# Kernel optimization log

Hardware: AMD Instinct MI355X
Metric: run time of the kernel (lower is better)

Reference implementation:

```python
import jax, jax.numpy as jnp
import numpy as np

N_NODES = 100000
N_EDGES = 1600000
N_GRAPHS = 2048
D = 128
H = 128
EPS = 1e-5


def gcn_conv(x, src, dst, W, b, n):
    # x: [N, Din], W: [Din, Dout]; GCN with added self-loops and symmetric norm
    xw = x @ W                                       # [N, Dout]
    deg = jnp.zeros((n,), x.dtype).at[dst].add(1.0) + 1.0  # deg of A+I (counted on dst)
    dinv = jax.lax.rsqrt(deg)                        # [N]
    norm = dinv[src] * dinv[dst]                     # [E]
    msg = xw[src] * norm[:, None]                    # [E, Dout] gather + scale
    agg = jax.ops.segment_sum(msg, dst, num_segments=n)
    agg = agg + xw * (dinv * dinv)[:, None]          # self-loop contribution
    return agg + b


def gru_step_h0(x, W_ih, W_hh, b_ih, b_hh):
    # single GRU step with h0 = 0 (PyTorch gate order r, z, n)
    h0 = jnp.zeros_like(x)
    gi = x @ W_ih.T + b_ih                           # [G, 3H]
    gh = h0 @ W_hh.T + b_hh                          # [G, 3H] (zeros + b_hh)
    ir, iz, inn = jnp.split(gi, 3, axis=-1)
    hr, hz, hn = jnp.split(gh, 3, axis=-1)
    r = jax.nn.sigmoid(ir + hr)
    z = jax.nn.sigmoid(iz + hz)
    n = jnp.tanh(inn + r * hn)
    return (1.0 - z) * n + z * h0


def setup_inputs() -> dict:
    key = jax.random.key(0)
    ks = jax.random.split(key, 10)
    x = jax.random.normal(ks[0], (N_NODES, D), jnp.float32)
    edge_index = jax.random.randint(ks[1], (2, N_EDGES), 0, N_NODES, jnp.int32)
    batch = jnp.sort(jax.random.randint(ks[2], (N_NODES,), 0, N_GRAPHS, jnp.int32))
    s = 1.0 / np.sqrt(H)
    return {
        "x": x,
        "edge_index": edge_index,
        "batch": batch,
        "W1": jax.random.normal(ks[3], (D, H), jnp.float32) * s,
        "b1": jnp.zeros((H,), jnp.float32),
        "W2": jax.random.normal(ks[4], (H, H), jnp.float32) * s,
        "b2": jnp.zeros((H,), jnp.float32),
        "W_ih": jax.random.normal(ks[5], (3 * H, H), jnp.float32) * s,
        "W_hh": jax.random.normal(ks[6], (3 * H, H), jnp.float32) * s,
        "b_ih": jnp.zeros((3 * H,), jnp.float32),
        "b_hh": jnp.zeros((3 * H,), jnp.float32),
        "W_lin": jax.random.normal(ks[7], (1, H), jnp.float32) * s,
        "b_lin": jnp.zeros((1,), jnp.float32),
    }


def reference(x, edge_index, batch, W1, b1, W2, b2, W_ih, W_hh, b_ih, b_hh, W_lin, b_lin):
    src, dst = edge_index[0], edge_index[1]
    n = x.shape[0]
    h = jax.nn.relu(gcn_conv(x, src, dst, W1, b1, n))
    h = gcn_conv(h, src, dst, W2, b2, n)
    # global_mean_pool over graph ids
    sums = jax.ops.segment_sum(h, batch, num_segments=N_GRAPHS)
    cnts = jax.ops.segment_sum(jnp.ones((n,), h.dtype), batch, num_segments=N_GRAPHS)
    g = sums / jnp.maximum(cnts, 1.0)[:, None]       # [G, H]
    # dropout p=0.5 in eval mode -> identity
    g = gru_step_h0(g, W_ih, W_hh, b_ih, b_hh)
    g = jax.nn.relu(g)
    mu = jnp.mean(g, axis=-1, keepdims=True)
    var = jnp.mean(jnp.square(g - mu), axis=-1, keepdims=True)
    g = (g - mu) * jax.lax.rsqrt(var + EPS)          # layer_norm, no affine
    return g @ W_lin.T + b_lin                       # [G, 1]
```

## Files before the change

kernel.cpp:

```cpp
#include <hip/hip_runtime.h>
#include <hip/hip_bf16.h>
#include <math.h>

#define DHID 128
#define SH 8
#define BIN_T 8192
#define CAPSH 13

typedef __attribute__((ext_vector_type(8))) short bf16x8;
typedef __attribute__((ext_vector_type(4))) float f32x4;

__device__ __forceinline__ int atomAddI(int* p, int v) {
    return __hip_atomic_fetch_add(p, v, __ATOMIC_RELAXED, __HIP_MEMORY_SCOPE_AGENT);
}
__device__ __forceinline__ float bf_lo(unsigned u) { return __uint_as_float(u << 16); }
__device__ __forceinline__ float bf_hi(unsigned u) { return __uint_as_float(u & 0xffff0000u); }
__device__ __forceinline__ float bf_us(unsigned short u) { return __uint_as_float((unsigned)u << 16); }
__device__ __forceinline__ unsigned short bf16_1(float f) {
    unsigned u = __float_as_uint(f);
    u += 0x7fffu + ((u >> 16) & 1u);
    return (unsigned short)(u >> 16);
}
__device__ __forceinline__ unsigned pack_bf16x2(float a, float b) {
    unsigned ua = __float_as_uint(a);
    unsigned ub = __float_as_uint(b);
    ua = (ua + 0x7fffu + ((ua >> 16) & 1u)) >> 16;
    ub = (ub + 0x7fffu + ((ub >> 16) & 1u)) & 0xffff0000u;
    return ua | ub;
}

__global__ __launch_bounds__(256) void bin_edges(const int* __restrict__ src,
                                                 const int* __restrict__ dst,
                                                 int* __restrict__ bcur,
                                                 unsigned* __restrict__ staged,
                                                 int E, int NB) {
    __shared__ int lh[512], lbase[512], lcur[512];
    int t = threadIdx.x;
    int e0 = blockIdx.x * BIN_T;
    int eend = min(e0 + BIN_T, E);
    for (int i = t; i < NB; i += 256) { lh[i] = 0; lcur[i] = 0; }
    __syncthreads();
    for (int e = e0 + t; e < eend; e += 256)
        atomicAdd(&lh[dst[e] >> SH], 1);
    __syncthreads();
    for (int i = t; i < NB; i += 256)
        lbase[i] = lh[i] ? atomAddI(&bcur[i], lh[i]) : 0;
    __syncthreads();
    for (int e = e0 + t; e < eend; e += 256) {
        int d = dst[e];
        int b = d >> SH;
        int pos = lbase[b] + atomicAdd(&lcur[b], 1);
        staged[((size_t)b << CAPSH) + pos] =
            (unsigned)src[e] | ((unsigned)(d & ((1 << SH) - 1)) << 24);
    }
}

__global__ __launch_bounds__(512) void scan_weights(const int* __restrict__ bcur,
                                                    int* __restrict__ gboff,
                                                    int* __restrict__ off,
                                                    const float* __restrict__ W1,
                                                    const float* __restrict__ W2,
                                                    const float* __restrict__ Wih,
                                                    unsigned short* __restrict__ Wt1,
                                                    unsigned short* __restrict__ Wt2,
                                                    unsigned short* __restrict__ Wihb,
                                                    int N, int E, int NB) {
    int t = threadIdx.x;
    if (blockIdx.x == 0) {
        __shared__ int sh[512];
        int v = (t < NB) ? bcur[t] : 0;
        sh[t] = v;
        __syncthreads();
#pragma unroll
        for (int o = 1; o < 512; o <<= 1) {
            int x = (t >= o) ? sh[t - o] : 0;
            __syncthreads();
            sh[t] += x;
            __syncthreads();
        }
        if (t < NB) gboff[t] = sh[t] - v;
        if (t == 0) { gboff[NB] = E; off[N] = E; }
    } else {
        int idx = (blockIdx.x - 1) * 512 + t;
        if (idx < 16384) {
            int k = idx >> 7, n = idx & 127;
            Wt1[n * 128 + k] = bf16_1(W1[idx]);
        } else if (idx < 32768) {
            int j = idx - 16384;
            int k = j >> 7, n = j & 127;
            Wt2[n * 128 + k] = bf16_1(W2[j]);
        } else if (idx < 32768 + 49152) {
            int j = idx - 32768;
            Wihb[j] = bf16_1(Wih[j]);
        }
    }
}

__global__ __launch_bounds__(256) void scatter_csr(const unsigned* __restrict__ staged,
                                                   const int* __restrict__ bcur,
                                                   const int* __restrict__ gboff,
                                                   int* __restrict__ off,
                                                   float* __restrict__ dinv,
                                                   int* __restrict__ rec, int N) {
    __shared__ int sh[256];
    __shared__ int curs[256];
    __shared__ int hist[256];
    int t = threadIdx.x;
    int b = blockIdx.x;
    int node0 = b << SH;
    int cnt_b = bcur[b];
    int base = gboff[b];
    const unsigned* st = staged + ((size_t)b << CAPSH);
    hist[t] = 0;
    __syncthreads();
    for (int j = t; j < cnt_b; j += 256)
        atomicAdd(&hist[st[j] >> 24], 1);
    __syncthreads();
    int v = hist[t];
    sh[t] = v;
    __syncthreads();
#pragma unroll
    for (int o = 1; o < 256; o <<= 1) {
        int x = (t >= o) ? sh[t - o] : 0;
        __syncthreads();
        sh[t] += x;
        __syncthreads();
    }
    int excl = sh[t] - v;
    int node = node0 + t;
    if (node < N) {
        off[node] = base + excl;
        dinv[node] = rsqrtf((float)v + 1.0f);
    }
    curs[t] = base + excl;
    __syncthreads();
    for (int j = t; j < cnt_b; j += 256) {
        unsigned w = st[j];
        int dl = w >> 24;
        int pos = atomicAdd(&curs[dl], 1);
        rec[pos] = (int)(w & 0xFFFFFFu);
    }
}

__global__ __launch_bounds__(256) void gemm_mfma(const void* __restrict__ Xv,
                                                 const unsigned short* __restrict__ Wt,
                                                 unsigned short* __restrict__ Y,
                                                 int N, int x_is_bf16,
                                                 int wstride, int ystride) {
    __shared__ unsigned short Xs[64 * 136];
    __shared__ unsigned short Ws[128 * 136];
    const int tid = threadIdx.x;
    const unsigned short* Wg = Wt + (size_t)blockIdx.y * wstride;
    unsigned short* Yg = Y + (size_t)blockIdx.y * ystride;

    {
        const uint4* W4 = (const uint4*)Wg;
#pragma unroll
        for (int i = 0; i < 8; i++) {
            int idx = tid + i * 256;
            int r = idx >> 4, c8 = idx & 15;
            *(uint4*)&Ws[r * 136 + c8 * 8] = W4[idx];
        }
    }
    const int row0 = blockIdx.x * 64;
    if (x_is_bf16) {
        const uint4* X4 = (const uint4*)Xv;
#pragma unroll
        for (int i = 0; i < 4; i++) {
            int idx = tid + i * 256;
            int r = idx >> 4, c8 = idx & 15;
            uint4 v = make_uint4(0u, 0u, 0u, 0u);
            if (row0 + r < N) v = X4[(size_t)(row0 + r) * 16 + c8];
            *(uint4*)&Xs[r * 136 + c8 * 8] = v;
        }
    } else {
        const float4* X4 = (const float4*)Xv;
#pragma unroll
        for (int i = 0; i < 8; i++) {
            int idx = tid + i * 256;
            int r = idx >> 5, c4 = idx & 31;
            float4 v = make_float4(0.f, 0.f, 0.f, 0.f);
            if (row0 + r < N) v = X4[(size_t)(row0 + r) * 32 + c4];
            uint2 pk = make_uint2(pack_bf16x2(v.x, v.y), pack_bf16x2(v.z, v.w));
            *(uint2*)&Xs[r * 136 + c4 * 4] = pk;
        }
    }
    __syncthreads();

    const int lane = tid & 63;
    const int wv = tid >> 6;
    const int m = lane & 15, quad = lane >> 4;
    const int wrow = wv * 16;

    f32x4 acc[8];
#pragma unroll
    for (int i = 0; i < 8; i++) acc[i] = (f32x4){0.f, 0.f, 0.f, 0.f};

#pragma unroll
    for (int kc = 0; kc < 4; kc++) {
        bf16x8 a = *(const bf16x8*)&Xs[(wrow + m) * 136 + kc * 32 + quad * 8];
#pragma unroll
        for (int nt = 0; nt < 8; nt++) {
            bf16x8 b = *(const bf16x8*)&Ws[(nt * 16 + m) * 136 + kc * 32 + quad * 8];
            acc[nt] = __builtin_amdgcn_mfma_f32_16x16x32_bf16(a, b, acc[nt], 0, 0, 0);
        }
    }

#pragma unroll
    for (int r = 0; r < 4; r++) {
        int row = row0 + wrow + quad * 4 + r;
        if (row < N) {
#pragma unroll
            for (int nt = 0; nt < 8; nt++) {
                Yg[(size_t)row * DHID + nt * 16 + m] = bf16_1(acc[nt][r]);
            }
        }
    }
}

__global__ __launch_bounds__(256) void aggregate(const unsigned short* __restrict__ A,
                                                 const float* __restrict__ dinv,
                                                 const int* __restrict__ off,
                                                 const int* __restrict__ rec,
                                                 const float* __restrict__ bias,
                                                 void* __restrict__ Bout, int N, int mode) {
    int node = blockIdx.x * 4 + (threadIdx.x >> 6);
    if (node >= N) return;
    int lane = threadIdx.x & 63;
    int q  = lane >> 4;
    int ql = lane & 15;
    float di = dinv[node];
    float acc[8];
    if (q == 0) {
        float s = di * di;
        uint4 v = ((const uint4*)(A + (size_t)node * DHID))[ql];
        const float4* bb = (const float4*)(bias + ql * 8);
        float4 b0 = bb[0], b1 = bb[1];
        acc[0] = bf_lo(v.x) * s + b0.x;
        acc[1] = bf_hi(v.x) * s + b0.y;
        acc[2] = bf_lo(v.y) * s + b0.z;
        acc[3] = bf_hi(v.y) * s + b0.w;
        acc[4] = bf_lo(v.z) * s + b1.x;
        acc[5] = bf_hi(v.z) * s + b1.y;
        acc[6] = bf_lo(v.w) * s + b1.z;
        acc[7] = bf_hi(v.w) * s + b1.w;
    } else {
#pragma unroll
        for (int i = 0; i < 8; i++) acc[i] = 0.f;
    }
    int j = off[node] + q;
    int jend = off[node + 1];
    for (; j + 4 < jend; j += 8) {
        int s0 = rec[j];
        int s1 = rec[j + 4];
        uint4 v0 = ((const uint4*)(A + (size_t)s0 * DHID))[ql];
        uint4 v1 = ((const uint4*)(A + (size_t)s1 * DHID))[ql];
        float w0 = dinv[s0] * di;
        float w1 = dinv[s1] * di;
        acc[0] += bf_lo(v0.x) * w0 + bf_lo(v1.x) * w1;
        acc[1] += bf_hi(v0.x) * w0 + bf_hi(v1.x) * w1;
        acc[2] += bf_lo(v0.y) * w0 + bf_lo(v1.y) * w1;
        acc[3] += bf_hi(v0.y) * w0 + bf_hi(v1.y) * w1;
        acc[4] += bf_lo(v0.z) * w0 + bf_lo(v1.z) * w1;
        acc[5] += bf_hi(v0.z) * w0 + bf_hi(v1.z) * w1;
        acc[6] += bf_lo(v0.w) * w0 + bf_lo(v1.w) * w1;
        acc[7] += bf_hi(v0.w) * w0 + bf_hi(v1.w) * w1;
    }
    if (j < jend) {
        int s0 = rec[j];
        uint4 v0 = ((const uint4*)(A + (size_t)s0 * DHID))[ql];
        float w0 = dinv[s0] * di;
        acc[0] += bf_lo(v0.x) * w0;
        acc[1] += bf_hi(v0.x) * w0;
        acc[2] += bf_lo(v0.y) * w0;
        acc[3] += bf_hi(v0.y) * w0;
        acc[4] += bf_lo(v0.z) * w0;
        acc[5] += bf_hi(v0.z) * w0;
        acc[6] += bf_lo(v0.w) * w0;
        acc[7] += bf_hi(v0.w) * w0;
    }
#pragma unroll
    for (int i = 0; i < 8; i++) {
        acc[i] += __shfl_xor(acc[i], 16);
        acc[i] += __shfl_xor(acc[i], 32);
    }
    if (q == 0) {
        if (mode == 1) {
            uint4 pk;
            pk.x = pack_bf16x2(fmaxf(acc[0], 0.f), fmaxf(acc[1], 0.f));
            pk.y = pack_bf16x2(fmaxf(acc[2], 0.f), fmaxf(acc[3], 0.f));
            pk.z = pack_bf16x2(fmaxf(acc[4], 0.f), fmaxf(acc[5], 0.f));
            pk.w = pack_bf16x2(fmaxf(acc[6], 0.f), fmaxf(acc[7], 0.f));
            ((uint4*)((unsigned short*)Bout + (size_t)node * DHID))[ql] = pk;
        } else {
            float4* bp = (float4*)((float*)Bout + (size_t)node * DHID) + ql * 2;
            bp[0] = make_float4(acc[0], acc[1], acc[2], acc[3]);
            bp[1] = make_float4(acc[4], acc[5], acc[6], acc[7]);
        }
    }
}

__global__ __launch_bounds__(256) void pool_mean(const float* __restrict__ B,
                                                 const int* __restrict__ batch,
                                                 float* __restrict__ g, int N, int G) {
    __shared__ int se[2];
    __shared__ float red[128];
    const int t = threadIdx.x;
    const int gr = blockIdx.x;
    if (t < 2) {
        int target = gr + t, lo = 0, hi = N;
        while (lo < hi) {
            int mid = (lo + hi) >> 1;
            if (batch[mid] < target) lo = mid + 1; else hi = mid;
        }
        se[t] = lo;
    }
    __syncthreads();
    const int s = se[0], e = se[1];
    const int col = t & 127, rh = t >> 7;
    float sum = 0.f;
    for (int r = s + rh; r < e; r += 2) sum += B[(size_t)r * DHID + col];
    if (rh == 1) red[col] = sum;
    __syncthreads();
    if (rh == 0) {
        float tot = sum + red[col];
        g[(size_t)gr * DHID + col] = tot / fmaxf((float)(e - s), 1.0f);
    }
}

__global__ __launch_bounds__(128) void gate_ln_head(const unsigned short* __restrict__ gi,
                                                    const float* __restrict__ b_ih,
                                                    const float* __restrict__ b_hh,
                                                    const float* __restrict__ W_lin,
                                                    const float* __restrict__ b_lin,
                                                    float* __restrict__ out, int G) {
    __shared__ float red[2];
    const int t = threadIdx.x;
    const int g = blockIdx.x;

    float d0 = bf_us(gi[(size_t)g * DHID + t]);
    float d1 = bf_us(gi[(size_t)(G + g) * DHID + t]);
    float d2 = bf_us(gi[(size_t)(2 * G + g) * DHID + t]);

    float rg = 1.f / (1.f + expf(-(d0 + b_ih[t] + b_hh[t])));
    float zg = 1.f / (1.f + expf(-(d1 + b_ih[128 + t] + b_hh[128 + t])));
    float ng = tanhf(d2 + b_ih[256 + t] + rg * b_hh[256 + t]);
    float y = fmaxf((1.f - zg) * ng, 0.f);

    auto blockSum = [&](float v) -> float {
#pragma unroll
        for (int o = 1; o < 64; o <<= 1) v += __shfl_xor(v, o);
        __syncthreads();
        if ((t & 63) == 0) red[t >> 6] = v;
        __syncthreads();
        return red[0] + red[1];
    };

    float mu = blockSum(y) * (1.f / 128.f);
    float dy = y - mu;
    float var = blockSum(dy * dy) * (1.f / 128.f);
    float yn = dy * rsqrtf(var + 1e-5f);
    float tot = blockSum(yn * W_lin[t]);
    if (t == 0) out[g] = tot + b_lin[0];
}

extern "C" void kernel_launch(void* const* d_in, const int* in_sizes, int n_in,
                              void* d_out, int out_size, void* d_ws, size_t ws_size,
                              hipStream_t stream) {
    const float* x     = (const float*)d_in[0];
    const int*   ei    = (const int*)d_in[1];
    const int*   batch = (const int*)d_in[2];
    const float* W1    = (const float*)d_in[3];
    const float* b1    = (const float*)d_in[4];
    const float* W2    = (const float*)d_in[5];
    const float* b2    = (const float*)d_in[6];
    const float* W_ih  = (const float*)d_in[7];
    const float* b_ih  = (const float*)d_in[9];
    const float* b_hh  = (const float*)d_in[10];
    const float* W_lin = (const float*)d_in[11];
    const float* b_lin = (const float*)d_in[12];
    float* out = (float*)d_out;

    const int N = in_sizes[0] / DHID;
    const int E = in_sizes[1] / 2;
    const int G = out_size;
    const int* src = ei;
    const int* dst = ei + E;
    const int NB = (N + (1 << SH) - 1) >> SH;

    auto align256 = [](size_t v) { return (v + 255) & ~(size_t)255; };
    char* p = (char*)d_ws;
    size_t used = 0;
    auto carve = [&](size_t bytes) -> char* {
        char* q = p + used;
        used += align256(bytes);
        return q;
    };

    int*   off    = (int*)carve(((size_t)N + 1) * 4);
    int*   bcur   = (int*)carve(512 * 4);
    int*   gboff  = (int*)carve(513 * 4);
    float* dinv   = (float*)carve((size_t)N * 4);
    unsigned* staged = (unsigned*)carve(((size_t)NB << CAPSH) * 4);
    int*   rec    = (int*)carve((size_t)E * 4);
    float* gbuf   = (float*)carve((size_t)G * DHID * 4);
    unsigned short* Wt1  = (unsigned short*)carve((size_t)128 * 128 * 2);
    unsigned short* Wt2  = (unsigned short*)carve((size_t)128 * 128 * 2);
    unsigned short* Wihb = (unsigned short*)carve((size_t)3 * 128 * 128 * 2);
    unsigned short* gib  = (unsigned short*)carve((size_t)3 * G * DHID * 2);
    unsigned short* A    = (unsigned short*)carve((size_t)N * DHID * 2);
    unsigned short* B1b  = (unsigned short*)carve((size_t)N * DHID * 2);
    size_t matB = (size_t)N * DHID * sizeof(float);
    float* B2f;
    if (ws_size >= used + matB) {
        B2f = (float*)carve(matB);
    } else {
        B2f = (float*)d_in[0];
    }

    dim3 blk(256);
    int nb_g  = (N + 63) / 64;
    int nb_ag = (N + 3) / 4;
    int nb_bin = (E + BIN_T - 1) / BIN_T;
    int nb_wp  = (81920 + 511) / 512;

    hipMemsetAsync(bcur, 0, (size_t)NB * 4, stream);
    bin_edges<<<nb_bin, blk, 0, stream>>>(src, dst, bcur, staged, E, NB);
    scan_weights<<<1 + nb_wp, dim3(512), 0, stream>>>(bcur, gboff, off,
                                                      W1, W2, W_ih, Wt1, Wt2, Wihb,
                                                      N, E, NB);
    scatter_csr<<<NB, blk, 0, stream>>>(staged, bcur, gboff, off, dinv, rec, N);

    gemm_mfma<<<dim3(nb_g, 1), blk, 0, stream>>>(x, Wt1, A, N, 0, 0, 0);
    aggregate<<<nb_ag, blk, 0, stream>>>(A, dinv, off, rec, b1, B1b, N, 1);

    gemm_mfma<<<dim3(nb_g, 1), blk, 0, stream>>>(B1b, Wt2, A, N, 1, 0, 0);
    aggregate<<<nb_ag, blk, 0, stream>>>(A, dinv, off, rec, b2, B2f, N, 0);

    pool_mean<<<G, blk, 0, stream>>>(B2f, batch, gbuf, N, G);
    gemm_mfma<<<dim3((G + 63) / 64, 3), blk, 0, stream>>>(gbuf, Wihb, gib, G, 0,
                                                          128 * 128, G * DHID);
    gate_ln_head<<<G, dim3(128), 0, stream>>>(gib, b_ih, b_hh, W_lin, b_lin, out, G);
}
```

Measured before the change: 364.7 us.

## Fuse bin/scan kernels, stage GEMM stores via LDS, store layer-2 output as bf16

```diff
diff --git a/kernel.cpp b/kernel.cpp
--- a/kernel.cpp
+++ b/kernel.cpp
@@ -33,55 +33,16 @@
                                                  const int* __restrict__ dst,
                                                  int* __restrict__ bcur,
                                                  unsigned* __restrict__ staged,
-                                                 int E, int NB) {
-    __shared__ int lh[512], lbase[512], lcur[512];
+                                                 const float* __restrict__ W1,
+                                                 const float* __restrict__ W2,
+                                                 const float* __restrict__ Wih,
+                                                 unsigned short* __restrict__ Wt1,
+                                                 unsigned short* __restrict__ Wt2,
+                                                 unsigned short* __restrict__ Wihb,
+                                                 int E, int NB, int nb_bin) {
     int t = threadIdx.x;
-    int e0 = blockIdx.x * BIN_T;
-    int eend = min(e0 + BIN_T, E);
-    for (int i = t; i < NB; i += 256) { lh[i] = 0; lcur[i] = 0; }
-    __syncthreads();
-    for (int e = e0 + t; e < eend; e += 256)
-        atomicAdd(&lh[dst[e] >> SH], 1);
-    __syncthreads();
-    for (int i = t; i < NB; i += 256)
-        lbase[i] = lh[i] ? atomAddI(&bcur[i], lh[i]) : 0;
-    __syncthreads();
-    for (int e = e0 + t; e < eend; e += 256) {
-        int d = dst[e];
-        int b = d >> SH;
-        int pos = lbase[b] + atomicAdd(&lcur[b], 1);
-        staged[((size_t)b << CAPSH) + pos] =
-            (unsigned)src[e] | ((unsigned)(d & ((1 << SH) - 1)) << 24);
-    }
-}
-
-__global__ __launch_bounds__(512) void scan_weights(const int* __restrict__ bcur,
-                                                    int* __restrict__ gboff,
-                                                    int* __restrict__ off,
-                                                    const float* __restrict__ W1,
-                                                    const float* __restrict__ W2,
-                                                    const float* __restrict__ Wih,
-                                                    unsigned short* __restrict__ Wt1,
-                                                    unsigned short* __restrict__ Wt2,
-                                                    unsigned short* __restrict__ Wihb,
-                                                    int N, int E, int NB) {
-    int t = threadIdx.x;
-    if (blockIdx.x == 0) {
-        __shared__ int sh[512];
-        int v = (t < NB) ? bcur[t] : 0;
-        sh[t] = v;
-        __syncthreads();
-#pragma unroll
-        for (int o = 1; o < 512; o <<= 1) {
-            int x = (t >= o) ? sh[t - o] : 0;
-            __syncthreads();
-            sh[t] += x;
-            __syncthreads();
-        }
-        if (t < NB) gboff[t] = sh[t] - v;
-        if (t == 0) { gboff[NB] = E; off[N] = E; }
-    } else {
-        int idx = (blockIdx.x - 1) * 512 + t;
+    if (blockIdx.x >= nb_bin) {
+        int idx = (blockIdx.x - nb_bin) * 256 + t;
         if (idx < 16384) {
             int k = idx >> 7, n = idx & 127;
             Wt1[n * 128 + k] = bf16_1(W1[idx]);
@@ -93,26 +54,55 @@
             int j = idx - 32768;
             Wihb[j] = bf16_1(Wih[j]);
         }
+        return;
+    }
+    __shared__ int lh[512], lbase[512], lcur[512];
+    int e0 = blockIdx.x * BIN_T;
+    int eend = min(e0 + BIN_T, E);
+    for (int i = t; i < NB; i += 256) { lh[i] = 0; lcur[i] = 0; }
+    __syncthreads();
+    for (int e = e0 + t; e < eend; e += 256)
+        atomicAdd(&lh[dst[e] >> SH], 1);
+    __syncthreads();
+    for (int i = t; i < NB; i += 256)
+        lbase[i] = lh[i] ? atomAddI(&bcur[i], lh[i]) : 0;
+    __syncthreads();
+    for (int e = e0 + t; e < eend; e += 256) {
+        int d = dst[e];
+        int b = d >> SH;
+        int pos = lbase[b] + atomicAdd(&lcur[b], 1);
+        staged[((size_t)b << CAPSH) + pos] =
+            (unsigned)src[e] | ((unsigned)(d & ((1 << SH) - 1)) << 24);
     }
 }
 
 __global__ __launch_bounds__(256) void scatter_csr(const unsigned* __restrict__ staged,
                                                    const int* __restrict__ bcur,
-                                                   const int* __restrict__ gboff,
                                                    int* __restrict__ off,
                                                    float* __restrict__ dinv,
-                                                   int* __restrict__ rec, int N) {
+                                                   int* __restrict__ rec,
+                                                   int N, int E, int NB) {
     __shared__ int sh[256];
     __shared__ int curs[256];
     __shared__ int hist[256];
     int t = threadIdx.x;
     int b = blockIdx.x;
     int node0 = b << SH;
+
+    int s0 = (t < b) ? bcur[t] : 0;
+    int s1 = (256 + t < b) ? bcur[256 + t] : 0;
+    int s = s0 + s1;
+#pragma unroll
+    for (int o = 1; o < 64; o <<= 1) s += __shfl_xor(s, o);
+    if ((t & 63) == 0) sh[t >> 6] = s;
+    __syncthreads();
+    int base = sh[0] + sh[1] + sh[2] + sh[3];
+    __syncthreads();
+
+    hist[t] = 0;
+    __syncthreads();
     int cnt_b = bcur[b];
-    int base = gboff[b];
     const unsigned* st = staged + ((size_t)b << CAPSH);
-    hist[t] = 0;
-    __syncthreads();
     for (int j = t; j < cnt_b; j += 256)
         atomicAdd(&hist[st[j] >> 24], 1);
     __syncthreads();
@@ -132,6 +122,7 @@
         off[node] = base + excl;
         dinv[node] = rsqrtf((float)v + 1.0f);
     }
+    if (b == NB - 1 && t == 0) off[N] = E;
     curs[t] = base + excl;
     __syncthreads();
     for (int j = t; j < cnt_b; j += 256) {
@@ -208,13 +199,19 @@
 
 #pragma unroll
     for (int r = 0; r < 4; r++) {
-        int row = row0 + wrow + quad * 4 + r;
-        if (row < N) {
-#pragma unroll
-            for (int nt = 0; nt < 8; nt++) {
-                Yg[(size_t)row * DHID + nt * 16 + m] = bf16_1(acc[nt][r]);
-            }
-        }
+        int lrow = wrow + quad * 4 + r;
+#pragma unroll
+        for (int nt = 0; nt < 8; nt++)
+            Xs[lrow * 136 + nt * 16 + m] = bf16_1(acc[nt][r]);
+    }
+    __syncthreads();
+#pragma unroll
+    for (int i = 0; i < 4; i++) {
+        int idx = tid + i * 256;
+        int r = idx >> 4, c8 = idx & 15;
+        if (row0 + r < N)
+            *(uint4*)&Yg[(size_t)(row0 + r) * DHID + c8 * 8] =
+                *(const uint4*)&Xs[r * 136 + c8 * 8];
     }
 }
 
@@ -223,7 +220,8 @@
                                                  const int* __restrict__ off,
                                                  const int* __restrict__ rec,
                                                  const float* __restrict__ bias,
-                                                 void* __restrict__ Bout, int N, int mode) {
+                                                 unsigned short* __restrict__ Bout,
+                                                 int N, int mode) {
     int node = blockIdx.x * 4 + (threadIdx.x >> 6);
     if (node >= N) return;
     int lane = threadIdx.x & 63;
@@ -286,21 +284,19 @@
     }
     if (q == 0) {
         if (mode == 1) {
-            uint4 pk;
-            pk.x = pack_bf16x2(fmaxf(acc[0], 0.f), fmaxf(acc[1], 0.f));
-            pk.y = pack_bf16x2(fmaxf(acc[2], 0.f), fmaxf(acc[3], 0.f));
-            pk.z = pack_bf16x2(fmaxf(acc[4], 0.f), fmaxf(acc[5], 0.f));
-            pk.w = pack_bf16x2(fmaxf(acc[6], 0.f), fmaxf(acc[7], 0.f));
-            ((uint4*)((unsigned short*)Bout + (size_t)node * DHID))[ql] = pk;
-        } else {
-            float4* bp = (float4*)((float*)Bout + (size_t)node * DHID) + ql * 2;
-            bp[0] = make_float4(acc[0], acc[1], acc[2], acc[3]);
-            bp[1] = make_float4(acc[4], acc[5], acc[6], acc[7]);
-        }
-    }
-}
-
-__global__ __launch_bounds__(256) void pool_mean(const float* __restrict__ B,
+#pragma unroll
+            for (int i = 0; i < 8; i++) acc[i] = fmaxf(acc[i], 0.f);
+        }
+        uint4 pk;
+        pk.x = pack_bf16x2(acc[0], acc[1]);
+        pk.y = pack_bf16x2(acc[2], acc[3]);
+        pk.z = pack_bf16x2(acc[4], acc[5]);
+        pk.w = pack_bf16x2(acc[6], acc[7]);
+        ((uint4*)(Bout + (size_t)node * DHID))[ql] = pk;
+    }
+}
+
+__global__ __launch_bounds__(256) void pool_mean(const unsigned short* __restrict__ B,
                                                  const int* __restrict__ batch,
                                                  float* __restrict__ g, int N, int G) {
     __shared__ int se[2];
@@ -319,7 +315,7 @@
     const int s = se[0], e = se[1];
     const int col = t & 127, rh = t >> 7;
     float sum = 0.f;
-    for (int r = s + rh; r < e; r += 2) sum += B[(size_t)r * DHID + col];
+    for (int r = s + rh; r < e; r += 2) sum += bf_us(B[(size_t)r * DHID + col]);
     if (rh == 1) red[col] = sum;
     __syncthreads();
     if (rh == 0) {
@@ -399,7 +395,6 @@
 
     int*   off    = (int*)carve(((size_t)N + 1) * 4);
     int*   bcur   = (int*)carve(512 * 4);
-    int*   gboff  = (int*)carve(513 * 4);
     float* dinv   = (float*)carve((size_t)N * 4);
     unsigned* staged = (unsigned*)carve(((size_t)NB << CAPSH) * 4);
     int*   rec    = (int*)carve((size_t)E * 4);
@@ -410,34 +405,33 @@
     unsigned short* gib  = (unsigned short*)carve((size_t)3 * G * DHID * 2);
     unsigned short* A    = (unsigned short*)carve((size_t)N * DHID * 2);
     unsigned short* B1b  = (unsigned short*)carve((size_t)N * DHID * 2);
-    size_t matB = (size_t)N * DHID * sizeof(float);
-    float* B2f;
+    size_t matB = (size_t)N * DHID * 2;
+    unsigned short* B2b;
     if (ws_size >= used + matB) {
-        B2f = (float*)carve(matB);
+        B2b = (unsigned short*)carve(matB);
     } else {
-        B2f = (float*)d_in[0];
+        B2b = (unsigned short*)d_in[0];
     }
 
     dim3 blk(256);
     int nb_g  = (N + 63) / 64;
     int nb_ag = (N + 3) / 4;
     int nb_bin = (E + BIN_T - 1) / BIN_T;
-    int nb_wp  = (81920 + 511) / 512;
+    int nb_wp  = (81920 + 255) / 256;
 
     hipMemsetAsync(bcur, 0, (size_t)NB * 4, stream);
-    bin_edges<<<nb_bin, blk, 0, stream>>>(src, dst, bcur, staged, E, NB);
-    scan_weights<<<1 + nb_wp, dim3(512), 0, stream>>>(bcur, gboff, off,
-                                                      W1, W2, W_ih, Wt1, Wt2, Wihb,
-                                                      N, E, NB);
-    scatter_csr<<<NB, blk, 0, stream>>>(staged, bcur, gboff, off, dinv, rec, N);
+    bin_edges<<<nb_bin + nb_wp, blk, 0, stream>>>(src, dst, bcur, staged,
+                                                  W1, W2, W_ih, Wt1, Wt2, Wihb,
+                                                  E, NB, nb_bin);
+    scatter_csr<<<NB, blk, 0, stream>>>(staged, bcur, off, dinv, rec, N, E, NB);
 
     gemm_mfma<<<dim3(nb_g, 1), blk, 0, stream>>>(x, Wt1, A, N, 0, 0, 0);
     aggregate<<<nb_ag, blk, 0, stream>>>(A, dinv, off, rec, b1, B1b, N, 1);
 
     gemm_mfma<<<dim3(nb_g, 1), blk, 0, stream>>>(B1b, Wt2, A, N, 1, 0, 0);
-    aggregate<<<nb_ag, blk, 0, stream>>>(A, dinv, off, rec, b2, B2f, N, 0);
-
-    pool_mean<<<G, blk, 0, stream>>>(B2f, batch, gbuf, N, G);
+    aggregate<<<nb_ag, blk, 0, stream>>>(A, dinv, off, rec, b2, B2b, N, 0);
+
+    pool_mean<<<G, blk, 0, stream>>>(B2b, batch, gbuf, N, G);
     gemm_mfma<<<dim3((G + 63) / 64, 3), blk, 0, stream>>>(gbuf, Wihb, gib, G, 0,
                                                           128 * 128, G * DHID);
     gate_ln_head<<<G, dim3(128), 0, stream>>>(gib, b_ih, b_hh, W_lin, b_lin, out, G);
```

After: 347.8 us. -4.6%, faster.
